# Kernel tuning notes

Hardware: AMD Instinct MI355X
Metric: run time of the kernel (lower is better)

## Reference

```python
import jax, jax.numpy as jnp
import numpy as np

C = 64
CK = C // 8  # query/key channels


def setup_inputs() -> dict:
    key = jax.random.key(0)
    ks = jax.random.split(key, 8)
    b, c, h, w = 4, C, 64, 64
    x = jax.random.normal(ks[0], (b, c, h, w), dtype=jnp.float32)
    # 1x1 conv weights (spectral-normalized weights are still just dense weights at eval)
    wq = jax.random.normal(ks[1], (CK, c), dtype=jnp.float32) * 0.05
    bq = jax.random.normal(ks[2], (CK,), dtype=jnp.float32) * 0.01
    wk = jax.random.normal(ks[3], (CK, c), dtype=jnp.float32) * 0.05
    bk = jax.random.normal(ks[4], (CK,), dtype=jnp.float32) * 0.01
    wv = jax.random.normal(ks[5], (c, c), dtype=jnp.float32) * 0.05
    bv = jax.random.normal(ks[6], (c,), dtype=jnp.float32) * 0.01
    # gamma is initialized to 0 in the module; use a nonzero value so the
    # attention path contributes to the output.
    gamma = jax.random.normal(ks[7], (1,), dtype=jnp.float32) * 0.5
    return {"x": x, "wq": wq, "bq": bq, "wk": wk, "bk": bk,
            "wv": wv, "bv": bv, "gamma": gamma}


def reference(x, wq, bq, wk, bk, wv, bv, gamma):
    b, c, h, w = x.shape
    n = h * w
    xf = x.reshape(b, c, n)                      # [b, c, n]
    # 1x1 convs as matmuls over the channel dim
    q = jnp.einsum('oc,bcn->bno', wq, xf) + bq   # [b, n, ck]
    k = jnp.einsum('oc,bcn->bon', wk, xf) + bk[None, :, None]  # [b, ck, n]
    v = jnp.einsum('oc,bcn->bno', wv, xf) + bv   # [b, n, c]
    attn = jax.nn.softmax(jnp.einsum('bnd,bdm->bnm', q, k), axis=-1)  # [b, n, n]
    o = jnp.einsum('bnm,bmc->bnc', attn, v)      # [b, n, c]
    o = o.transpose(0, 2, 1).reshape(b, c, h, w)
    return gamma[0] * o + x
```

## Files before the change

### kernel.cpp

```cpp
#include <hip/hip_runtime.h>
#include <hip/hip_bf16.h>

#define CH 64
#define NN 4096
#define NB 4
#define SPLIT 4
#define KLEN (NN / SPLIT)
#define PHK 512
#define VSTRIDE 520
#define LOG2E 1.44269504f

typedef unsigned short u16;
typedef unsigned int u32;
typedef __attribute__((ext_vector_type(8))) short bf16x8;
typedef __attribute__((ext_vector_type(16))) float f32x16;

static __device__ __forceinline__ u16 bf16r(float f) {
  union { float f; unsigned u; } v; v.f = f;
  unsigned x = v.u;
  x += 0x7fffu + ((x >> 16) & 1u);
  return (u16)(x >> 16);
}
static __device__ __forceinline__ u32 pkc(float a, float b) {
  union { __hip_bfloat162 h; u32 u; } r;
  r.h = __float22bfloat162_rn(float2{a, b});
  return r.u;
}

__global__ __launch_bounds__(192) void prep_w(
    const float* __restrict__ wq, const float* __restrict__ wk,
    const float* __restrict__ wv, u16* __restrict__ Afr) {
  for (int idx = threadIdx.x; idx < 768; idx += 192) {
    const int l = idx & 63;
    const int s = (idx >> 6) & 3;
    const int t = idx >> 8;
    const int row = 32 * t + (l & 31);
    const int c0 = 16 * s + 8 * (l >> 5);
    float e[8];
#pragma unroll
    for (int j = 0; j < 8; ++j) {
      float v = 0.f;
      if (row < 64)      v = wv[row * 64 + c0 + j];
      else if (row < 72) v = wq[(row - 64) * 64 + c0 + j];
      else if (row < 80) v = wk[(row - 72) * 64 + c0 + j];
      e[j] = v;
    }
    u32* dst = reinterpret_cast<u32*>(Afr + (size_t)idx * 8);
    dst[0] = pkc(e[0], e[1]); dst[1] = pkc(e[2], e[3]);
    dst[2] = pkc(e[4], e[5]); dst[3] = pkc(e[6], e[7]);
  }
}

__global__ __launch_bounds__(192) void qkv_proj(
    const float* __restrict__ x, const u16* __restrict__ Afr,
    const float* __restrict__ bq, const float* __restrict__ bk,
    const float* __restrict__ bv,
    u16* __restrict__ Qb, u16* __restrict__ Kb, u16* __restrict__ Vb) {
  __shared__ float xs[64 * 32];
  const int tid = threadIdx.x;
  const int b = blockIdx.x >> 7;
  const int n0 = (blockIdx.x & 127) << 5;

  const float* xbase = x + (size_t)b * CH * NN + n0;
  for (int i = tid; i < 512; i += 192) {
    const int row = i >> 3, c4 = i & 7;
    *reinterpret_cast<float4*>(&xs[row * 32 + c4 * 4]) =
        *reinterpret_cast<const float4*>(xbase + (size_t)row * NN + c4 * 4);
  }
  __syncthreads();

  const int w = __builtin_amdgcn_readfirstlane(tid >> 6);
  const int lane = tid & 63;
  const int l31 = lane & 31;
  const int h = lane >> 5;
  const int n = n0 + l31;

  f32x16 acc = {};
#pragma unroll
  for (int s = 0; s < 4; ++s) {
    const bf16x8 af = *reinterpret_cast<const bf16x8*>(
        Afr + ((size_t)(w * 4 + s) * 64 + lane) * 8);
    float xv[8];
#pragma unroll
    for (int j = 0; j < 8; ++j)
      xv[j] = xs[(16 * s + 8 * h + j) * 32 + l31];
    union { uint4 u; bf16x8 v; } bf;
    bf.u.x = pkc(xv[0], xv[1]); bf.u.y = pkc(xv[2], xv[3]);
    bf.u.z = pkc(xv[4], xv[5]); bf.u.w = pkc(xv[6], xv[7]);
    acc = __builtin_amdgcn_mfma_f32_32x32x16_bf16(af, bf.v, acc, 0, 0, 0);
  }

  if (w < 2) {
    const int sperm = (l31 & 19) | ((l31 & 4) << 1) | ((l31 & 8) >> 1);
    const int nperm = n0 + sperm;
#pragma unroll
    for (int r = 0; r < 16; ++r) {
      const int row = 32 * w + (r & 3) + 8 * (r >> 2) + 4 * h;
      Vb[((size_t)b * CH + row) * NN + nperm] = bf16r(acc[r] + bv[row]);
    }
  } else {
    const float q0 = (acc[0] + bq[4 * h + 0]) * LOG2E;
    const float q1 = (acc[1] + bq[4 * h + 1]) * LOG2E;
    const float q2 = (acc[2] + bq[4 * h + 2]) * LOG2E;
    const float q3 = (acc[3] + bq[4 * h + 3]) * LOG2E;
    const float k0 = acc[4] + bk[4 * h + 0];
    const float k1 = acc[5] + bk[4 * h + 1];
    const float k2 = acc[6] + bk[4 * h + 2];
    const float k3 = acc[7] + bk[4 * h + 3];
    uint2 qv, kv;
    qv.x = pkc(q0, q1); qv.y = pkc(q2, q3);
    kv.x = pkc(k0, k1); kv.y = pkc(k2, k3);
    *reinterpret_cast<uint2*>(Qb + ((size_t)b * NN + n) * 8 + 4 * h) = qv;
    *reinterpret_cast<uint2*>(Kb + ((size_t)b * NN + n) * 8 + 4 * h) = kv;
  }
}

__global__ __launch_bounds__(512, 4) void flash_attn(
    const u16* __restrict__ Qb, const u16* __restrict__ Kb,
    const u16* __restrict__ Vb, u32* __restrict__ ACCu,
    float* __restrict__ Lb) {
  __shared__ u16 Klds[PHK * 8 + 8];
  __shared__ u16 Vlds[64 * VSTRIDE];
  const int bid = blockIdx.x;
  const int sp = bid & 3;
  const int rest = bid >> 2;
  const int qc = rest & 15;
  const int b = rest >> 4;
  const int w = __builtin_amdgcn_readfirstlane(threadIdx.x >> 6);
  const int lane = threadIdx.x & 63;
  const int l31 = lane & 31;
  const int h = lane >> 5;
  const int qrow0 = qc * 256 + w * 32;
  const int ks = sp * KLEN;

  if (threadIdx.x < 8) Klds[PHK * 8 + threadIdx.x] = 0;

  bf16x8 qf = {0, 0, 0, 0, 0, 0, 0, 0};
  if (h == 0)
    qf = *reinterpret_cast<const bf16x8*>(Qb + ((size_t)b * NN + qrow0 + l31) * 8);

  const u16* Kp = Kb + ((size_t)b * NN + ks) * 8;
  const u16* Vp = Vb + (size_t)b * CH * NN + ks;

  f32x16 acc0 = {}, acc1 = {}, acc2 = {};
  const f32x16 zz = {};
  const short one = (short)0x3F80;
  const bf16x8 zero8 = {0, 0, 0, 0, 0, 0, 0, 0};
  const bf16x8 ones8 = {one, one, one, one, one, one, one, one};
  const bf16x8 af1 = (l31 == 0) ? ones8 : zero8;
  const int m0 = (l31 ^ (l31 >> 3)) & 7;
  const int m1 = m0 ^ 4;

#define STAGE(ph) do {                                                        \
    _Pragma("unroll")                                                         \
    for (int i = 0; i < 8; ++i) {                                             \
      const int ch = 8 * w + i;                                               \
      const int mm = (ch ^ (ch >> 3)) & 7;                                    \
      const u16* src = Vp + (size_t)ch * NN + (ph) * PHK +                    \
                       (((lane & 56) | ((lane ^ mm) & 7)) << 3);              \
      __builtin_amdgcn_global_load_lds(                                       \
          (const __attribute__((address_space(1))) void*)src,                 \
          (__attribute__((address_space(3))) void*)&Vlds[ch * VSTRIDE], 16, 0, 0); \
    }                                                                         \
    __builtin_amdgcn_global_load_lds(                                         \
        (const __attribute__((address_space(1))) void*)(Kp + ((size_t)(ph) * PHK + 64 * w + lane) * 8), \
        (__attribute__((address_space(3))) void*)&Klds[64 * w * 8], 16, 0, 0); \
  } while (0)

#pragma unroll
  for (int ph = 0; ph < 2; ++ph) {
    STAGE(ph);
    __syncthreads();
#pragma unroll 4
    for (int kk = 0; kk < PHK / 32; ++kk) {
      const int kaddr = h ? PHK * 8 : (kk * 32 + l31) * 8;
      bf16x8 kf = *reinterpret_cast<const bf16x8*>(Klds + kaddr);
      f32x16 s = __builtin_amdgcn_mfma_f32_32x32x16_bf16(kf, qf, zz, 0, 0, 0);
      float p[16];
#pragma unroll
      for (int r = 0; r < 16; ++r) p[r] = exp2f(s[r]);
      union { uint4 u; bf16x8 v; } pb0, pb1;
      pb0.u.x = pkc(p[0], p[1]);   pb0.u.y = pkc(p[2], p[3]);
      pb0.u.z = pkc(p[4], p[5]);   pb0.u.w = pkc(p[6], p[7]);
      pb1.u.x = pkc(p[8], p[9]);   pb1.u.y = pkc(p[10], p[11]);
      pb1.u.z = pkc(p[12], p[13]); pb1.u.w = pkc(p[14], p[15]);
      const int g0 = kk * 4 + h;
      const int g1 = g0 + 2;
      const int cp00 = (g0 & 56) | ((g0 ^ m0) & 7);
      const int cp01 = (g1 & 56) | ((g1 ^ m0) & 7);
      const int cp10 = (g0 & 56) | ((g0 ^ m1) & 7);
      const int cp11 = (g1 & 56) | ((g1 ^ m1) & 7);
      bf16x8 v00 = *reinterpret_cast<const bf16x8*>(Vlds + l31 * VSTRIDE + cp00 * 8);
      bf16x8 v01 = *reinterpret_cast<const bf16x8*>(Vlds + l31 * VSTRIDE + cp01 * 8);
      bf16x8 v10 = *reinterpret_cast<const bf16x8*>(Vlds + (32 + l31) * VSTRIDE + cp10 * 8);
      bf16x8 v11 = *reinterpret_cast<const bf16x8*>(Vlds + (32 + l31) * VSTRIDE + cp11 * 8);
      acc0 = __builtin_amdgcn_mfma_f32_32x32x16_bf16(v00, pb0.v, acc0, 0, 0, 0);
      acc0 = __builtin_amdgcn_mfma_f32_32x32x16_bf16(v01, pb1.v, acc0, 0, 0, 0);
      acc1 = __builtin_amdgcn_mfma_f32_32x32x16_bf16(v10, pb0.v, acc1, 0, 0, 0);
      acc1 = __builtin_amdgcn_mfma_f32_32x32x16_bf16(v11, pb1.v, acc1, 0, 0, 0);
      acc2 = __builtin_amdgcn_mfma_f32_32x32x16_bf16(af1, pb0.v, acc2, 0, 0, 0);
      acc2 = __builtin_amdgcn_mfma_f32_32x32x16_bf16(af1, pb1.v, acc2, 0, 0, 0);
    }
    if (ph == 0) __syncthreads();
  }
#undef STAGE

  float lsum = acc2[0];
  lsum += __shfl_xor(lsum, 32);

  const int gtile = b * (NN / 32) + qc * 8 + w;
  u32* A = ACCu + ((size_t)gtile * SPLIT + sp) * 32 * 32;
#pragma unroll
  for (int rp = 0; rp < 8; ++rp) {
    const int chp = (rp & 1) + 4 * (rp >> 1) + 2 * h;
    __builtin_nontemporal_store(pkc(acc0[2 * rp], acc0[2 * rp + 1]),
                                &A[chp * 32 + l31]);
    __builtin_nontemporal_store(pkc(acc1[2 * rp], acc1[2 * rp + 1]),
                                &A[(16 + chp) * 32 + l31]);
  }
  if (h == 0)
    __builtin_nontemporal_store(lsum, &Lb[((size_t)gtile * SPLIT + sp) * 32 + l31]);
}

__global__ __launch_bounds__(256) void combine(
    const float* __restrict__ x, const float* __restrict__ gamma,
    const u32* __restrict__ ACCu, const float* __restrict__ Lb,
    float* __restrict__ out) {
  const int idx = blockIdx.x * 256 + threadIdx.x;
  const int n4 = idx & (NN / 4 - 1);
  const int cp = (idx >> 10) & 31;
  const int b = idx >> 15;
  const int n = n4 << 2;
  const int gtile = b * (NN / 32) + (n >> 5);
  const int q0 = n & 31;
  const uint4* A4 = reinterpret_cast<const uint4*>(ACCu);
  const float4* L4 = reinterpret_cast<const float4*>(Lb);
  float s0[4] = {0.f, 0.f, 0.f, 0.f}, s1[4] = {0.f, 0.f, 0.f, 0.f};
  float l[4] = {0.f, 0.f, 0.f, 0.f};
#pragma unroll
  for (int sp = 0; sp < SPLIT; ++sp) {
    const uint4 a = A4[(((size_t)gtile * SPLIT + sp) * 32 + cp) * 8 + (q0 >> 2)];
    const float4 lv = L4[(((size_t)gtile * SPLIT + sp) * 32 + q0) >> 2];
    const u32 av[4] = {a.x, a.y, a.z, a.w};
#pragma unroll
    for (int k = 0; k < 4; ++k) {
      union { u32 u; float f; } lo, hi;
      lo.u = av[k] << 16; hi.u = av[k] & 0xffff0000u;
      s0[k] += lo.f; s1[k] += hi.f;
    }
    l[0] += lv.x; l[1] += lv.y; l[2] += lv.z; l[3] += lv.w;
  }
  const float gm = gamma[0];
  float inv[4];
#pragma unroll
  for (int k = 0; k < 4; ++k) inv[k] = gm / l[k];
  const size_t i0 = ((size_t)b * CH + 2 * cp) * NN + n;
  const float4 x0 = *reinterpret_cast<const float4*>(x + i0);
  const float4 x1 = *reinterpret_cast<const float4*>(x + i0 + NN);
  float4 o0, o1;
  o0.x = fmaf(inv[0], s0[0], x0.x); o0.y = fmaf(inv[1], s0[1], x0.y);
  o0.z = fmaf(inv[2], s0[2], x0.z); o0.w = fmaf(inv[3], s0[3], x0.w);
  o1.x = fmaf(inv[0], s1[0], x1.x); o1.y = fmaf(inv[1], s1[1], x1.y);
  o1.z = fmaf(inv[2], s1[2], x1.z); o1.w = fmaf(inv[3], s1[3], x1.w);
  *reinterpret_cast<float4*>(out + i0) = o0;
  *reinterpret_cast<float4*>(out + i0 + NN) = o1;
}

extern "C" void kernel_launch(void* const* d_in, const int* in_sizes, int n_in,
                              void* d_out, int out_size, void* d_ws, size_t ws_size,
                              hipStream_t stream) {
  const float* x     = (const float*)d_in[0];
  const float* wq    = (const float*)d_in[1];
  const float* bq    = (const float*)d_in[2];
  const float* wk    = (const float*)d_in[3];
  const float* bk    = (const float*)d_in[4];
  const float* wv    = (const float*)d_in[5];
  const float* bv    = (const float*)d_in[6];
  const float* gamma = (const float*)d_in[7];
  float* out = (float*)d_out;

  u16* Qb = (u16*)d_ws;
  u16* Kb = Qb + (size_t)NB * NN * 8;
  u16* Vb = Kb + (size_t)NB * NN * 8;
  u32* ACCu = (u32*)(Vb + (size_t)NB * CH * NN);
  float* Lb = (float*)(ACCu + (size_t)NB * (NN / 32) * SPLIT * 32 * 32);
  u16* Afr = (u16*)(Lb + (size_t)NB * (NN / 32) * SPLIT * 32);

  prep_w<<<dim3(1), dim3(192), 0, stream>>>(wq, wk, wv, Afr);
  qkv_proj<<<dim3(NB * (NN / 32)), dim3(192), 0, stream>>>(
      x, Afr, bq, bk, bv, Qb, Kb, Vb);
  flash_attn<<<dim3(NB * 16 * SPLIT), dim3(512), 0, stream>>>(
      Qb, Kb, Vb, ACCu, Lb);
  combine<<<dim3((NB * 32 * (NN / 4)) / 256), dim3(256), 0, stream>>>(
      x, gamma, ACCu, Lb, out);
}
```

Baseline: 112.4 us.

## Double-buffer K/V staging in flash attention and fold weight prep into projection

The flash attention kernel now splits each key chunk into four 256-key phases held in two LDS buffers, issuing the async load of the next phase while computing the current one. Phase order is rotated per query chunk to spread memory traffic. The separate prep_w launch is removed: each qkv_proj block builds the bf16 weight fragments in LDS itself. This trades fewer launches and overlapped loads for redundant per-block weight conversion and more barriers.

Result: no change. 111.6 us (-0.6%).

```diff
diff --git a/kernel.cpp b/kernel.cpp
--- a/kernel.cpp
+++ b/kernel.cpp
@@ -6,8 +6,9 @@
 #define NB 4
 #define SPLIT 4
 #define KLEN (NN / SPLIT)
-#define PHK 512
-#define VSTRIDE 520
+#define PHK 256
+#define NP (KLEN / PHK)
+#define VST 256
 #define LOG2E 1.44269504f
 
 typedef unsigned short u16;
@@ -27,13 +28,28 @@
   return r.u;
 }
 
-__global__ __launch_bounds__(192) void prep_w(
-    const float* __restrict__ wq, const float* __restrict__ wk,
-    const float* __restrict__ wv, u16* __restrict__ Afr) {
-  for (int idx = threadIdx.x; idx < 768; idx += 192) {
-    const int l = idx & 63;
-    const int s = (idx >> 6) & 3;
-    const int t = idx >> 8;
+__global__ __launch_bounds__(192) void qkv_proj(
+    const float* __restrict__ x,
+    const float* __restrict__ wq, const float* __restrict__ bq,
+    const float* __restrict__ wk, const float* __restrict__ bk,
+    const float* __restrict__ wv, const float* __restrict__ bv,
+    u16* __restrict__ Qb, u16* __restrict__ Kb, u16* __restrict__ Vb) {
+  __shared__ float xs[64 * 32];
+  __shared__ u16 afr_lds[3][4][64][8];
+  const int tid = threadIdx.x;
+  const int b = blockIdx.x >> 7;
+  const int n0 = (blockIdx.x & 127) << 5;
+
+  const float* xbase = x + (size_t)b * CH * NN + n0;
+  for (int i = tid; i < 512; i += 192) {
+    const int row = i >> 3, c4 = i & 7;
+    *reinterpret_cast<float4*>(&xs[row * 32 + c4 * 4]) =
+        *reinterpret_cast<const float4*>(xbase + (size_t)row * NN + c4 * 4);
+  }
+  for (int i = tid; i < 768; i += 192) {
+    const int l = i & 63;
+    const int s = (i >> 6) & 3;
+    const int t = i >> 8;
     const int row = 32 * t + (l & 31);
     const int c0 = 16 * s + 8 * (l >> 5);
     float e[8];
@@ -45,27 +61,9 @@
       else if (row < 80) v = wk[(row - 72) * 64 + c0 + j];
       e[j] = v;
     }
-    u32* dst = reinterpret_cast<u32*>(Afr + (size_t)idx * 8);
+    u32* dst = reinterpret_cast<u32*>(&afr_lds[t][s][l][0]);
     dst[0] = pkc(e[0], e[1]); dst[1] = pkc(e[2], e[3]);
     dst[2] = pkc(e[4], e[5]); dst[3] = pkc(e[6], e[7]);
-  }
-}
-
-__global__ __launch_bounds__(192) void qkv_proj(
-    const float* __restrict__ x, const u16* __restrict__ Afr,
-    const float* __restrict__ bq, const float* __restrict__ bk,
-    const float* __restrict__ bv,
-    u16* __restrict__ Qb, u16* __restrict__ Kb, u16* __restrict__ Vb) {
-  __shared__ float xs[64 * 32];
-  const int tid = threadIdx.x;
-  const int b = blockIdx.x >> 7;
-  const int n0 = (blockIdx.x & 127) << 5;
-
-  const float* xbase = x + (size_t)b * CH * NN + n0;
-  for (int i = tid; i < 512; i += 192) {
-    const int row = i >> 3, c4 = i & 7;
-    *reinterpret_cast<float4*>(&xs[row * 32 + c4 * 4]) =
-        *reinterpret_cast<const float4*>(xbase + (size_t)row * NN + c4 * 4);
   }
   __syncthreads();
 
@@ -78,8 +76,7 @@
   f32x16 acc = {};
 #pragma unroll
   for (int s = 0; s < 4; ++s) {
-    const bf16x8 af = *reinterpret_cast<const bf16x8*>(
-        Afr + ((size_t)(w * 4 + s) * 64 + lane) * 8);
+    const bf16x8 af = *reinterpret_cast<const bf16x8*>(&afr_lds[w][s][lane][0]);
     float xv[8];
 #pragma unroll
     for (int j = 0; j < 8; ++j)
@@ -119,8 +116,8 @@
     const u16* __restrict__ Qb, const u16* __restrict__ Kb,
     const u16* __restrict__ Vb, u32* __restrict__ ACCu,
     float* __restrict__ Lb) {
-  __shared__ u16 Klds[PHK * 8 + 8];
-  __shared__ u16 Vlds[64 * VSTRIDE];
+  __shared__ u16 Klds[2][PHK * 8 + 8];
+  __shared__ u16 Vlds[2][64 * VST];
   const int bid = blockIdx.x;
   const int sp = bid & 3;
   const int rest = bid >> 2;
@@ -132,8 +129,12 @@
   const int h = lane >> 5;
   const int qrow0 = qc * 256 + w * 32;
   const int ks = sp * KLEN;
-
-  if (threadIdx.x < 8) Klds[PHK * 8 + threadIdx.x] = 0;
+  const int rot = qc & 3;
+
+  if (threadIdx.x < 8) {
+    Klds[0][PHK * 8 + threadIdx.x] = 0;
+    Klds[1][PHK * 8 + threadIdx.x] = 0;
+  }
 
   bf16x8 qf = {0, 0, 0, 0, 0, 0, 0, 0};
   if (h == 0)
@@ -141,6 +142,28 @@
 
   const u16* Kp = Kb + ((size_t)b * NN + ks) * 8;
   const u16* Vp = Vb + (size_t)b * CH * NN + ks;
+
+  size_t vsrc[4];
+#pragma unroll
+  for (int i = 0; i < 4; ++i) {
+    const int ch = 8 * w + 2 * i + (lane >> 5);
+    const int mm = (ch ^ (ch >> 3)) & 7;
+    const int c = lane & 31;
+    vsrc[i] = (size_t)ch * NN + (size_t)((((c & 24) | ((c ^ mm) & 7)) << 3));
+  }
+
+#define STAGE(php, bb) do {                                                   \
+    const int kofs_ = (php) * PHK;                                            \
+    _Pragma("unroll")                                                         \
+    for (int i_ = 0; i_ < 4; ++i_)                                            \
+      __builtin_amdgcn_global_load_lds(                                       \
+          (const __attribute__((address_space(1))) void*)(Vp + vsrc[i_] + kofs_), \
+          (__attribute__((address_space(3))) void*)&Vlds[bb][(8 * w + 2 * i_) * VST], 16, 0, 0); \
+    if (w < 4)                                                                \
+      __builtin_amdgcn_global_load_lds(                                       \
+          (const __attribute__((address_space(1))) void*)(Kp + (size_t)(kofs_ + 64 * w + lane) * 8), \
+          (__attribute__((address_space(3))) void*)&Klds[bb][64 * w * 8], 16, 0, 0); \
+  } while (0)
 
   f32x16 acc0 = {}, acc1 = {}, acc2 = {};
   const f32x16 zz = {};
@@ -151,30 +174,16 @@
   const int m0 = (l31 ^ (l31 >> 3)) & 7;
   const int m1 = m0 ^ 4;
 
-#define STAGE(ph) do {                                                        \
-    _Pragma("unroll")                                                         \
-    for (int i = 0; i < 8; ++i) {                                             \
-      const int ch = 8 * w + i;                                               \
-      const int mm = (ch ^ (ch >> 3)) & 7;                                    \
-      const u16* src = Vp + (size_t)ch * NN + (ph) * PHK +                    \
-                       (((lane & 56) | ((lane ^ mm) & 7)) << 3);              \
-      __builtin_amdgcn_global_load_lds(                                       \
-          (const __attribute__((address_space(1))) void*)src,                 \
-          (__attribute__((address_space(3))) void*)&Vlds[ch * VSTRIDE], 16, 0, 0); \
-    }                                                                         \
-    __builtin_amdgcn_global_load_lds(                                         \
-        (const __attribute__((address_space(1))) void*)(Kp + ((size_t)(ph) * PHK + 64 * w + lane) * 8), \
-        (__attribute__((address_space(3))) void*)&Klds[64 * w * 8], 16, 0, 0); \
-  } while (0)
-
-#pragma unroll
-  for (int ph = 0; ph < 2; ++ph) {
-    STAGE(ph);
-    __syncthreads();
+  STAGE(rot, 0);
+  __syncthreads();
+#pragma unroll
+  for (int i = 0; i < NP; ++i) {
+    const int bb = i & 1;
+    if (i + 1 < NP) STAGE((rot + i + 1) & 3, bb ^ 1);
 #pragma unroll 4
     for (int kk = 0; kk < PHK / 32; ++kk) {
       const int kaddr = h ? PHK * 8 : (kk * 32 + l31) * 8;
-      bf16x8 kf = *reinterpret_cast<const bf16x8*>(Klds + kaddr);
+      bf16x8 kf = *reinterpret_cast<const bf16x8*>(&Klds[bb][kaddr]);
       f32x16 s = __builtin_amdgcn_mfma_f32_32x32x16_bf16(kf, qf, zz, 0, 0, 0);
       float p[16];
 #pragma unroll
@@ -186,14 +195,14 @@
       pb1.u.z = pkc(p[12], p[13]); pb1.u.w = pkc(p[14], p[15]);
       const int g0 = kk * 4 + h;
       const int g1 = g0 + 2;
-      const int cp00 = (g0 & 56) | ((g0 ^ m0) & 7);
-      const int cp01 = (g1 & 56) | ((g1 ^ m0) & 7);
-      const int cp10 = (g0 & 56) | ((g0 ^ m1) & 7);
-      const int cp11 = (g1 & 56) | ((g1 ^ m1) & 7);
-      bf16x8 v00 = *reinterpret_cast<const bf16x8*>(Vlds + l31 * VSTRIDE + cp00 * 8);
-      bf16x8 v01 = *reinterpret_cast<const bf16x8*>(Vlds + l31 * VSTRIDE + cp01 * 8);
-      bf16x8 v10 = *reinterpret_cast<const bf16x8*>(Vlds + (32 + l31) * VSTRIDE + cp10 * 8);
-      bf16x8 v11 = *reinterpret_cast<const bf16x8*>(Vlds + (32 + l31) * VSTRIDE + cp11 * 8);
+      const int cp00 = (g0 & 24) | ((g0 ^ m0) & 7);
+      const int cp01 = (g1 & 24) | ((g1 ^ m0) & 7);
+      const int cp10 = (g0 & 24) | ((g0 ^ m1) & 7);
+      const int cp11 = (g1 & 24) | ((g1 ^ m1) & 7);
+      bf16x8 v00 = *reinterpret_cast<const bf16x8*>(&Vlds[bb][l31 * VST + cp00 * 8]);
+      bf16x8 v01 = *reinterpret_cast<const bf16x8*>(&Vlds[bb][l31 * VST + cp01 * 8]);
+      bf16x8 v10 = *reinterpret_cast<const bf16x8*>(&Vlds[bb][(32 + l31) * VST + cp10 * 8]);
+      bf16x8 v11 = *reinterpret_cast<const bf16x8*>(&Vlds[bb][(32 + l31) * VST + cp11 * 8]);
       acc0 = __builtin_amdgcn_mfma_f32_32x32x16_bf16(v00, pb0.v, acc0, 0, 0, 0);
       acc0 = __builtin_amdgcn_mfma_f32_32x32x16_bf16(v01, pb1.v, acc0, 0, 0, 0);
       acc1 = __builtin_amdgcn_mfma_f32_32x32x16_bf16(v10, pb0.v, acc1, 0, 0, 0);
@@ -201,7 +210,7 @@
       acc2 = __builtin_amdgcn_mfma_f32_32x32x16_bf16(af1, pb0.v, acc2, 0, 0, 0);
       acc2 = __builtin_amdgcn_mfma_f32_32x32x16_bf16(af1, pb1.v, acc2, 0, 0, 0);
     }
-    if (ph == 0) __syncthreads();
+    __syncthreads();
   }
 #undef STAGE
 
@@ -284,11 +293,9 @@
   u16* Vb = Kb + (size_t)NB * NN * 8;
   u32* ACCu = (u32*)(Vb + (size_t)NB * CH * NN);
   float* Lb = (float*)(ACCu + (size_t)NB * (NN / 32) * SPLIT * 32 * 32);
-  u16* Afr = (u16*)(Lb + (size_t)NB * (NN / 32) * SPLIT * 32);
-
-  prep_w<<<dim3(1), dim3(192), 0, stream>>>(wq, wk, wv, Afr);
+
   qkv_proj<<<dim3(NB * (NN / 32)), dim3(192), 0, stream>>>(
-      x, Afr, bq, bk, bv, Qb, Kb, Vb);
+      x, wq, bq, wk, bk, wv, bv, Qb, Kb, Vb);
   flash_attn<<<dim3(NB * 16 * SPLIT), dim3(512), 0, stream>>>(
       Qb, Kb, Vb, ACCu, Lb);
   combine<<<dim3((NB * 32 * (NN / 4)) / 256), dim3(256), 0, stream>>>(
```
